# Kernel tuning notes

Hardware: AMD Instinct MI355X
Metric: run time of the kernel (lower is better)

## Reference

```python
import jax, jax.numpy as jnp
import numpy as np

DT = 0.019999999552965164
G = 9.8100004196167
GEAR = 100.0
B = 4_194_304


def setup_inputs() -> dict:
    key = jax.random.key(0)
    ks = jax.random.split(key, 5)
    f32 = jnp.float32
    inp = {
        "x": jax.random.normal(ks[0], (B, 1), f32),
        "v": jax.random.normal(ks[1], (B, 1), f32),
        "theta": jax.random.normal(ks[2], (B, 1), f32),
        "omega": jax.random.normal(ks[3], (B, 1), f32),
        "u": jax.random.normal(ks[4], (B, 1), f32),
        # learned physical parameters (values from the traced checkpoint)
        "I": jnp.array([0.33061733841896057], f32),
        "b": jnp.array([0.9297953844070435], f32),
        "d": jnp.array([1.0003730058670044], f32),
        "l": jnp.array([0.20579937100410461], f32),
        "m1": jnp.array([8.182073593139648], f32),
        "m2": jnp.array([7.310985088348389], f32),
    }
    return inp


def _cartpole_step(x, v, theta, omega, u, I, b, d, l, m1, m2):
    """One RK4 step of cart-pole dynamics (states x, v, theta, omega)."""
    F = GEAR * u
    M = m1 + m2
    Ieff = I + m2 * l * l  # effective pendulum inertia about pivot

    def deriv(s):
        x_, v_, th, om = s
        sin_t = jnp.sin(th)
        cos_t = jnp.cos(th)
        # coupled EOM:
        #  M*xdd + m2*l*cos(th)*thdd = F - b*v + m2*l*om^2*sin(th)
        #  Ieff*thdd + m2*l*cos(th)*xdd = m2*g*l*sin(th) - d*om
        A = F - b * v_ + m2 * l * om * om * sin_t
        Bq = m2 * G * l * sin_t - d * om
        ml_c = m2 * l * cos_t
        D = Ieff * M - ml_c * ml_c
        xdd = (Ieff * A - ml_c * Bq) / D
        thdd = (M * Bq - ml_c * A) / D
        return (v_, xdd, om, thdd)

    s0 = (x, v, theta, omega)
    half = DT / 2.0
    k1 = deriv(s0)
    k2 = deriv(jax.tree.map(lambda s, k: s + half * k, s0, k1))
    k3 = deriv(jax.tree.map(lambda s, k: s + half * k, s0, k2))
    k4 = deriv(jax.tree.map(lambda s, k: s + DT * k, s0, k3))
    nxt = jax.tree.map(
        lambda s, a, bb, c, e: s + (DT / 6.0) * (a + 2.0 * bb + 2.0 * c + e),
        s0, k1, k2, k3, k4,
    )
    return jnp.concatenate(nxt, axis=-1)  # [B, 4] = (x, v, theta, omega) next


def reference(x, v, theta, omega, u, I, b, d, l, m1, m2):
    return _cartpole_step(x, v, theta, omega, u, I, b, d, l, m1, m2)
```

## Files before the change

### kernel.cpp

```cpp
#include <hip/hip_runtime.h>
#include <math.h>

#define DT    0.019999999552965164f
#define GRAV  9.8100004196167f
#define GEAR  100.0f

typedef float vfloat4 __attribute__((ext_vector_type(4)));

__global__ __launch_bounds__(256) void cartpole_rk4_kernel(
    const float* __restrict__ x,
    const float* __restrict__ v,
    const float* __restrict__ th,
    const float* __restrict__ om,
    const float* __restrict__ u,
    const float* __restrict__ pI,
    const float* __restrict__ pb,
    const float* __restrict__ pd,
    const float* __restrict__ pl,
    const float* __restrict__ pm1,
    const float* __restrict__ pm2,
    vfloat4* __restrict__ out,
    int n)
{
    int i = blockIdx.x * blockDim.x + threadIdx.x;
    if (i >= n) return;

    const float I  = pI[0];
    const float b  = pb[0];
    const float d  = pd[0];
    const float l  = pl[0];
    const float m1 = pm1[0];
    const float m2 = pm2[0];

    const float M     = m1 + m2;
    const float m2l   = m2 * l;
    const float Ieff  = I + m2l * l;
    const float m2gl  = m2l * GRAV;
    const float IeffM = Ieff * M;

    const float x0 = x[i];
    const float v0 = v[i];
    const float t0 = th[i];
    const float o0 = om[i];
    const float F  = GEAR * u[i];

    auto deriv = [&](float v_, float t_, float o_, float& xdd, float& tdd) {
        float s, c;
        __sincosf(t_, &s, &c);
        float A    = F - b * v_ + m2l * o_ * o_ * s;
        float Bq   = m2gl * s - d * o_;
        float mlc  = m2l * c;
        float D    = IeffM - mlc * mlc;
        float invD = __builtin_amdgcn_rcpf(D);
        xdd = (Ieff * A - mlc * Bq) * invD;
        tdd = (M * Bq - mlc * A) * invD;
    };

    const float half = 0.5f * DT;

    float k1v, k1o;
    deriv(v0, t0, o0, k1v, k1o);

    float v2 = v0 + half * k1v;
    float t2 = t0 + half * o0;
    float o2 = o0 + half * k1o;
    float k2v, k2o;
    deriv(v2, t2, o2, k2v, k2o);

    float v3 = v0 + half * k2v;
    float t3 = t0 + half * o2;
    float o3 = o0 + half * k2o;
    float k3v, k3o;
    deriv(v3, t3, o3, k3v, k3o);

    float v4 = v0 + DT * k3v;
    float t4 = t0 + DT * o3;
    float o4 = o0 + DT * k3o;
    float k4v, k4o;
    deriv(v4, t4, o4, k4v, k4o);

    const float w = DT * (1.0f / 6.0f);

    vfloat4 r;
    r.x = x0 + w * (v0  + 2.0f * v2  + 2.0f * v3  + v4);
    r.y = v0 + w * (k1v + 2.0f * k2v + 2.0f * k3v + k4v);
    r.z = t0 + w * (o0  + 2.0f * o2  + 2.0f * o3  + o4);
    r.w = o0 + w * (k1o + 2.0f * k2o + 2.0f * k3o + k4o);

    __builtin_nontemporal_store(r, out + i);
}

extern "C" void kernel_launch(void* const* d_in, const int* in_sizes, int n_in,
                              void* d_out, int out_size, void* d_ws, size_t ws_size,
                              hipStream_t stream) {
    const float* x   = (const float*)d_in[0];
    const float* v   = (const float*)d_in[1];
    const float* th  = (const float*)d_in[2];
    const float* om  = (const float*)d_in[3];
    const float* u   = (const float*)d_in[4];
    const float* pI  = (const float*)d_in[5];
    const float* pb  = (const float*)d_in[6];
    const float* pd  = (const float*)d_in[7];
    const float* pl  = (const float*)d_in[8];
    const float* pm1 = (const float*)d_in[9];
    const float* pm2 = (const float*)d_in[10];

    int n = in_sizes[0];
    vfloat4* out = (vfloat4*)d_out;

    int block = 256;
    int grid = (n + block - 1) / block;
    cartpole_rk4_kernel<<<grid, block, 0, stream>>>(
        x, v, th, om, u, pI, pb, pd, pl, pm1, pm2, out, n);
}
```

Before: 28.32 us.

## Process four elements per thread with vector loads and LDS-transposed coalesced stores

Each thread now loads float4 vectors from the five input arrays and integrates four consecutive elements, cutting the grid to a quarter of the previous size. Results are staged in shared memory and transposed so each store instruction writes contiguous 16-byte outputs across the block. The goal is fewer, wider memory transactions and more work per thread to amortise parameter loads. The cost is a block barrier, 16KB of LDS per block, more registers per thread, and dropping the nontemporal store hint.

```diff
diff --git a/kernel.cpp b/kernel.cpp
--- a/kernel.cpp
+++ b/kernel.cpp
@@ -7,43 +7,11 @@
 
 typedef float vfloat4 __attribute__((ext_vector_type(4)));
 
-__global__ __launch_bounds__(256) void cartpole_rk4_kernel(
-    const float* __restrict__ x,
-    const float* __restrict__ v,
-    const float* __restrict__ th,
-    const float* __restrict__ om,
-    const float* __restrict__ u,
-    const float* __restrict__ pI,
-    const float* __restrict__ pb,
-    const float* __restrict__ pd,
-    const float* __restrict__ pl,
-    const float* __restrict__ pm1,
-    const float* __restrict__ pm2,
-    vfloat4* __restrict__ out,
-    int n)
+__device__ __forceinline__ void rk4_one(
+    float x0, float v0, float t0, float o0, float F,
+    float b, float d, float M, float m2l, float Ieff, float m2gl, float IeffM,
+    vfloat4& r)
 {
-    int i = blockIdx.x * blockDim.x + threadIdx.x;
-    if (i >= n) return;
-
-    const float I  = pI[0];
-    const float b  = pb[0];
-    const float d  = pd[0];
-    const float l  = pl[0];
-    const float m1 = pm1[0];
-    const float m2 = pm2[0];
-
-    const float M     = m1 + m2;
-    const float m2l   = m2 * l;
-    const float Ieff  = I + m2l * l;
-    const float m2gl  = m2l * GRAV;
-    const float IeffM = Ieff * M;
-
-    const float x0 = x[i];
-    const float v0 = v[i];
-    const float t0 = th[i];
-    const float o0 = om[i];
-    const float F  = GEAR * u[i];
-
     auto deriv = [&](float v_, float t_, float o_, float& xdd, float& tdd) {
         float s, c;
         __sincosf(t_, &s, &c);
@@ -80,14 +48,80 @@
     deriv(v4, t4, o4, k4v, k4o);
 
     const float w = DT * (1.0f / 6.0f);
-
-    vfloat4 r;
     r.x = x0 + w * (v0  + 2.0f * v2  + 2.0f * v3  + v4);
     r.y = v0 + w * (k1v + 2.0f * k2v + 2.0f * k3v + k4v);
     r.z = t0 + w * (o0  + 2.0f * o2  + 2.0f * o3  + o4);
     r.w = o0 + w * (k1o + 2.0f * k2o + 2.0f * k3o + k4o);
+}
 
-    __builtin_nontemporal_store(r, out + i);
+__global__ __launch_bounds__(256) void cartpole_rk4_kernel(
+    const float* __restrict__ x,
+    const float* __restrict__ v,
+    const float* __restrict__ th,
+    const float* __restrict__ om,
+    const float* __restrict__ u,
+    const float* __restrict__ pI,
+    const float* __restrict__ pb,
+    const float* __restrict__ pd,
+    const float* __restrict__ pl,
+    const float* __restrict__ pm1,
+    const float* __restrict__ pm2,
+    vfloat4* __restrict__ out,
+    int n)
+{
+    __shared__ vfloat4 sm[1024];
+
+    const float I  = pI[0];
+    const float b  = pb[0];
+    const float d  = pd[0];
+    const float l  = pl[0];
+    const float m1 = pm1[0];
+    const float m2 = pm2[0];
+
+    const float M     = m1 + m2;
+    const float m2l   = m2 * l;
+    const float Ieff  = I + m2l * l;
+    const float m2gl  = m2l * GRAV;
+    const float IeffM = Ieff * M;
+
+    const int tid  = threadIdx.x;
+    const int base = blockIdx.x * 1024;
+    const int i0   = base + tid * 4;
+
+    if (base + 1023 < n) {
+        const vfloat4 xv = *reinterpret_cast<const vfloat4*>(x  + i0);
+        const vfloat4 vv = *reinterpret_cast<const vfloat4*>(v  + i0);
+        const vfloat4 tv = *reinterpret_cast<const vfloat4*>(th + i0);
+        const vfloat4 ov = *reinterpret_cast<const vfloat4*>(om + i0);
+        const vfloat4 uv = *reinterpret_cast<const vfloat4*>(u  + i0);
+
+        vfloat4 r0, r1, r2, r3;
+        rk4_one(xv.x, vv.x, tv.x, ov.x, GEAR * uv.x, b, d, M, m2l, Ieff, m2gl, IeffM, r0);
+        rk4_one(xv.y, vv.y, tv.y, ov.y, GEAR * uv.y, b, d, M, m2l, Ieff, m2gl, IeffM, r1);
+        rk4_one(xv.z, vv.z, tv.z, ov.z, GEAR * uv.z, b, d, M, m2l, Ieff, m2gl, IeffM, r2);
+        rk4_one(xv.w, vv.w, tv.w, ov.w, GEAR * uv.w, b, d, M, m2l, Ieff, m2gl, IeffM, r3);
+
+        sm[0 * 256 + tid] = r0;
+        sm[1 * 256 + tid] = r1;
+        sm[2 * 256 + tid] = r2;
+        sm[3 * 256 + tid] = r3;
+
+        __syncthreads();
+
+#pragma unroll
+        for (int j = 0; j < 4; ++j) {
+            int e = 256 * j + tid;
+            vfloat4 r = sm[(e & 3) * 256 + (e >> 2)];
+            out[base + e] = r;
+        }
+    } else {
+        for (int i = i0; i < n && i < i0 + 4; ++i) {
+            vfloat4 r;
+            rk4_one(x[i], v[i], th[i], om[i], GEAR * u[i],
+                    b, d, M, m2l, Ieff, m2gl, IeffM, r);
+            out[i] = r;
+        }
+    }
 }
 
 extern "C" void kernel_launch(void* const* d_in, const int* in_sizes, int n_in,
@@ -109,7 +143,8 @@
     vfloat4* out = (vfloat4*)d_out;
 
     int block = 256;
-    int grid = (n + block - 1) / block;
+    int elems_per_block = block * 4;
+    int grid = (n + elems_per_block - 1) / elems_per_block;
     cartpole_rk4_kernel<<<grid, block, 0, stream>>>(
         x, v, th, om, u, pI, pb, pd, pl, pm1, pm2, out, n);
 }
```

Result: slower. 31.21 us (+10.2%).
